# Optimization experiments

Hardware: AMD Instinct MI355X
Metric: run time of the kernel (lower is better)

Reference implementation:

```python
import jax, jax.numpy as jnp
import numpy as np

N = 2048
H_DIM = 64
N_HEADS = 4
N_HIDDEN = H_DIM // N_HEADS  # is_concat=True
L = 16  # max_labels_dim
SLOPE = 0.2


def leaky(x, slope=SLOPE):
    return jnp.where(x >= 0, x, slope * x)


def setup_inputs() -> dict:
    key = jax.random.key(0)
    k1, k2, k3, k4 = jax.random.split(key, 4)
    x = jax.random.normal(k1, (N, H_DIM), dtype=jnp.float32)
    # labels in [0, L]; value == L means unlabeled -> all-zero one-hot row
    lab = jax.random.randint(k2, (N,), 0, L + 1)
    ohm_labels = jnp.where((lab < L)[:, None],
                           jax.nn.one_hot(jnp.minimum(lab, L - 1), L, dtype=jnp.float32),
                           0.0)
    in_features = H_DIM + L
    W_l = jax.random.normal(k3, (H_DIM, in_features), dtype=jnp.float32) / np.sqrt(in_features)
    W_attn = jax.random.normal(k4, (N_HIDDEN,), dtype=jnp.float32) / np.sqrt(N_HIDDEN)
    return {"x": x, "ohm_labels": ohm_labels, "W_l": W_l, "W_attn": W_attn, "sparsity": 0}


def reference(x, ohm_labels, W_l, W_attn, sparsity):
    n_nodes = x.shape[0]
    # fill unlabeled rows with uniform 1/L
    unlabeled = ohm_labels.sum(axis=1) == 0  # (N,)
    ohm = jnp.where(unlabeled[:, None], 1.0 / L, ohm_labels)
    pin = jnp.concatenate([x, ohm], axis=1)  # (N, h_dim + L)

    # shared-weight projection: g_l == g_r == g
    g = (pin @ W_l.T).reshape(n_nodes, N_HEADS, N_HIDDEN)  # (N, H, F)
    # g_sum[i, j] = g_l[j] + g_r[i]  (repeat / repeat_interleave semantics)
    g_sum = g[None, :, :, :] + g[:, None, :, :]            # (N, N, H, F)
    e = jnp.einsum('ijhf,f->ijh', leaky(g_sum), W_attn)    # (N, N, H)
    a = jax.nn.softmax(e, axis=1)                          # softmax over j
    # dropout in eval mode: identity
    attn_res = jnp.einsum('ijh,jhf->ihf', a, g)            # (N, H, F)
    out = attn_res.reshape(n_nodes, N_HEADS * N_HIDDEN)    # is_concat
    h = leaky(out)                                         # processor activation

    # centroids per label from ohm (post-fill) as in get_centroids
    cluster_agg = ohm.T @ h                                # (L, D)
    cnt = ohm.sum(axis=0)                                  # (L,)
    missing = cnt == 0
    centroids = jnp.where(missing[:, None], 0.0,
                          cluster_agg / jnp.where(missing, 1.0, cnt)[:, None])
    # cdist p=2
    diff = h[:, None, :] - centroids[None, :, :]           # (N, L, D)
    scores = -jnp.sqrt(jnp.sum(diff * diff, axis=-1))      # (N, L)
    return scores, h, missing
```

## Files before the change

### kernel.cpp

```cpp
#include <hip/hip_runtime.h>
#include <hip/hip_bf16.h>
#include <math.h>

#define C1F  0.577078016f
#define C2F  0.865617024f

#define WS_CNT 0
#define WS_AGG 128
#define WS_G   8320
#define WS_DCL (8320 + 524288)

typedef float __attribute__((ext_vector_type(4))) f32x4;

__device__ __forceinline__ float rfl(float x) {
    return __uint_as_float(__builtin_amdgcn_readfirstlane(__float_as_uint(x)));
}

__device__ __forceinline__ float dpp_sum(float x) {
    float y;
    y = __int_as_float(__builtin_amdgcn_update_dpp(0, __float_as_int(x), 0x111, 0xf, 0xf, true)); x += y;
    y = __int_as_float(__builtin_amdgcn_update_dpp(0, __float_as_int(x), 0x112, 0xf, 0xf, true)); x += y;
    y = __int_as_float(__builtin_amdgcn_update_dpp(0, __float_as_int(x), 0x114, 0xf, 0xf, true)); x += y;
    y = __int_as_float(__builtin_amdgcn_update_dpp(0, __float_as_int(x), 0x118, 0xf, 0xf, true)); x += y;
    y = __int_as_float(__builtin_amdgcn_update_dpp(0, __float_as_int(x), 0x142, 0xa, 0xf, true)); x += y;
    y = __int_as_float(__builtin_amdgcn_update_dpp(0, __float_as_int(x), 0x143, 0xc, 0xf, true)); x += y;
    return x;
}

__global__ __launch_bounds__(256) void k_proj(
    const float* __restrict__ x, const float* __restrict__ ohm,
    const float* __restrict__ Wl, const float* __restrict__ Wattn,
    unsigned char* __restrict__ ws)
{
    float* g    = (float*)(ws + WS_G);
    float* dclT = (float*)(ws + WS_DCL);
    unsigned long long* cnt = (unsigned long long*)(ws + WS_CNT);

    int t = threadIdx.x;
    int r = blockIdx.x * 4 + (t >> 6);
    int o = t & 63;

    f32x4 oh[4]; float rs = 0.f;
    const f32x4* ohp = (const f32x4*)&ohm[r*16];
    #pragma unroll
    for (int q = 0; q < 4; ++q) { oh[q] = ohp[q]; rs += oh[q][0]+oh[q][1]+oh[q][2]+oh[q][3]; }
    if (rs == 0.f) {
        f32x4 c = {0.0625f, 0.0625f, 0.0625f, 0.0625f};
        #pragma unroll
        for (int q = 0; q < 4; ++q) oh[q] = c;
    }

    float acc = 0.f;
    const f32x4* xp = (const f32x4*)&x[r*64];
    const f32x4* wp = (const f32x4*)&Wl[o*80];
    #pragma unroll
    for (int q = 0; q < 16; ++q) {
        f32x4 a = xp[q], b = wp[q];
        acc = fmaf(a[0],b[0],acc); acc = fmaf(a[1],b[1],acc);
        acc = fmaf(a[2],b[2],acc); acc = fmaf(a[3],b[3],acc);
    }
    #pragma unroll
    for (int q = 0; q < 4; ++q) {
        f32x4 b = wp[16+q];
        acc = fmaf(oh[q][0],b[0],acc); acc = fmaf(oh[q][1],b[1],acc);
        acc = fmaf(oh[q][2],b[2],acc); acc = fmaf(oh[q][3],b[3],acc);
    }
    g[r*64 + o] = acc;

    float dot = Wattn[o & 15] * acc;
    #pragma unroll
    for (int m2 = 1; m2 < 16; m2 <<= 1) dot += __shfl_xor(dot, m2);
    if ((o & 15) == 0) dclT[(o >> 4)*2048 + r] = C2F * dot;

    if (t < 16) {
        float c = 0.f;
        for (int rr = 0; rr < 4; ++rr) {
            int r2 = blockIdx.x*4 + rr; float s = 0.f;
            #pragma unroll
            for (int k = 0; k < 16; ++k) s += ohm[r2*16+k];
            c += (s == 0.f) ? 0.0625f : ohm[r2*16+t];
        }
        atomicAdd(&cnt[t], (unsigned long long)__float2ll_rn(c * 1048576.0f));
    }
}

__global__ __launch_bounds__(512, 3) void k_attn(
    const float* __restrict__ ohm, const float* __restrict__ Wattn,
    unsigned char* __restrict__ ws, float* __restrict__ hout)
{
    float* g    = (float*)(ws + WS_G);
    float* dclT = (float*)(ws + WS_DCL);
    unsigned long long* agg = (unsigned long long*)(ws + WS_AGG);

    __shared__ float gl[128*68];
    __shared__ float shh[256];
    __shared__ float ohmf[64];

    int t = threadIdx.x, bid = blockIdx.x;
    int wid = t >> 6, l = t & 63;
    int rp = wid >> 2, h = wid & 3;
    int i0 = bid*4 + rp*2, i1 = i0 + 1;

    const f32x4* gv4 = (const f32x4*)g;
    float* wbase = &gl[(t >> 4)*68 + (t & 15)*4];

    float wv[16], gA0[16], gA1[16];
    #pragma unroll
    for (int f = 0; f < 16; ++f) wv[f] = rfl(Wattn[f]);
    #pragma unroll
    for (int f = 0; f < 16; ++f) {
        gA0[f] = rfl(g[i0*64 + h*16 + f]);
        gA1[f] = rfl(g[i1*64 + h*16 + f]);
    }

    float acc0[16], acc1[16];
    float l0 = 0.f, l1 = 0.f;
    #pragma unroll
    for (int f = 0; f < 16; ++f) { acc0[f] = 0.f; acc1[f] = 0.f; }

    const float* dpt = dclT + h*2048 + l;

    f32x4 st[4];
    #pragma unroll
    for (int q = 0; q < 4; ++q) st[q] = gv4[t + q*512];
    float djc0 = dpt[0], djc1 = dpt[64];
    float djn0 = 0.f, djn1 = 0.f;

    for (int tile = 0; tile < 16; ++tile) {
        if (tile) __syncthreads();
        #pragma unroll
        for (int q = 0; q < 4; ++q) *(f32x4*)(wbase + q*2176) = st[q];
        __syncthreads();
        if (tile < 15) {
            #pragma unroll
            for (int q = 0; q < 4; ++q) st[q] = gv4[(tile+1)*2048 + t + q*512];
            djn0 = dpt[(tile+1)*128];
            djn1 = dpt[(tile+1)*128 + 64];
        }

        #pragma unroll
        for (int k = 0; k < 2; ++k) {
            const float* gj = &gl[(k*64 + l)*68 + h*16];
            f32x4 q0 = *(const f32x4*)(gj);
            f32x4 q1 = *(const f32x4*)(gj+4);
            f32x4 q2 = *(const f32x4*)(gj+8);
            f32x4 q3 = *(const f32x4*)(gj+12);
            float gvv[16] = { q0[0],q0[1],q0[2],q0[3], q1[0],q1[1],q1[2],q1[3],
                              q2[0],q2[1],q2[2],q2[3], q3[0],q3[1],q3[2],q3[3] };
            float sa0 = 0.f, sb0 = 0.f, sa1 = 0.f, sb1 = 0.f;
            #pragma unroll
            for (int f = 0; f < 16; f += 2) {
                float u0 = gA0[f]   + gvv[f];
                float u1 = gA0[f+1] + gvv[f+1];
                float v0 = gA1[f]   + gvv[f];
                float v1 = gA1[f+1] + gvv[f+1];
                sa0 = fmaf(wv[f],   fabsf(u0), sa0);
                sb0 = fmaf(wv[f+1], fabsf(u1), sb0);
                sa1 = fmaf(wv[f],   fabsf(v0), sa1);
                sb1 = fmaf(wv[f+1], fabsf(v1), sb1);
            }
            float djk = k ? djc1 : djc0;
            float p0 = __builtin_amdgcn_exp2f(fmaf(C1F, sa0 + sb0, djk));
            float p1 = __builtin_amdgcn_exp2f(fmaf(C1F, sa1 + sb1, djk));
            l0 += p0; l1 += p1;
            #pragma unroll
            for (int f = 0; f < 16; ++f) {
                acc0[f] = fmaf(p0, gvv[f], acc0[f]);
                acc1[f] = fmaf(p1, gvv[f], acc1[f]);
            }
        }
        djc0 = djn0; djc1 = djn1;
    }

    float ls0 = dpp_sum(l0), ls1 = dpp_sum(l1);
    float h0[16], h1[16];
    #pragma unroll
    for (int f = 0; f < 16; ++f) { h0[f] = dpp_sum(acc0[f]); h1[f] = dpp_sum(acc1[f]); }

    if (l == 63) {
        float r0 = 1.0f / ls0, r1 = 1.0f / ls1;
        #pragma unroll
        for (int f = 0; f < 16; ++f) {
            float a = h0[f]*r0; a = fmaxf(a, 0.2f*a);
            float b = h1[f]*r1; b = fmaxf(b, 0.2f*b);
            hout[i0*64 + h*16 + f] = a;
            hout[i1*64 + h*16 + f] = b;
            shh[(rp*2    )*64 + h*16 + f] = a;
            shh[(rp*2 + 1)*64 + h*16 + f] = b;
        }
    }
    if (t < 64) {
        int rr = t >> 4, ll = t & 15;
        float v = ohm[(bid*4 + rr)*16 + ll];
        float s = v;
        #pragma unroll
        for (int m2 = 1; m2 < 16; m2 <<= 1) s += __shfl_xor(s, m2);
        ohmf[rr*16 + ll] = (s == 0.f) ? 0.0625f : v;
    }
    __syncthreads();

    for (int v = t; v < 1024; v += 512) {
        int ll = v >> 6, d = v & 63;
        float s = 0.f;
        #pragma unroll
        for (int rr = 0; rr < 4; ++rr) s = fmaf(ohmf[rr*16 + ll], shh[rr*64 + d], s);
        atomicAdd(&agg[v], (unsigned long long)__float2ll_rn(s * 67108864.0f));
    }
}

__global__ __launch_bounds__(256) void k_scores(
    unsigned char* __restrict__ ws, const float* __restrict__ hout,
    float* __restrict__ scores, float* __restrict__ missing)
{
    __shared__ float cl[16*68];
    unsigned long long* cnt = (unsigned long long*)(ws + WS_CNT);
    unsigned long long* agg = (unsigned long long*)(ws + WS_AGG);
    int t = threadIdx.x;

    for (int v = t; v < 1024; v += 256) {
        int ll = v >> 6, d = v & 63;
        long long a = (long long)agg[v];
        long long c = (long long)cnt[ll];
        cl[ll*68 + d] = (c == 0) ? 0.f : ((float)a / (float)c) * 0.015625f;
    }
    if (blockIdx.x == 0 && t < 16) missing[t] = (cnt[t] == 0) ? 1.0f : 0.0f;
    __syncthreads();

    int i = blockIdx.x*16 + (t >> 4), ll = t & 15;
    float s = 0.f;
    #pragma unroll 16
    for (int d = 0; d < 64; ++d) {
        float diff = hout[i*64 + d] - cl[ll*68 + d];
        s = fmaf(diff, diff, s);
    }
    scores[i*16 + ll] = -sqrtf(s);
}

extern "C" void kernel_launch(void* const* d_in, const int* in_sizes, int n_in,
                              void* d_out, int out_size, void* d_ws, size_t ws_size,
                              hipStream_t stream)
{
    const float* x     = (const float*)d_in[0];
    const float* ohm   = (const float*)d_in[1];
    const float* Wl    = (const float*)d_in[2];
    const float* Wattn = (const float*)d_in[3];
    unsigned char* ws  = (unsigned char*)d_ws;

    float* out     = (float*)d_out;
    float* scores  = out;
    float* hout    = out + 2048*16;
    float* missing = out + 2048*16 + 2048*64;

    hipMemsetAsync(d_ws, 0, 8320, stream);
    k_proj  <<<512, 256, 0, stream>>>(x, ohm, Wl, Wattn, ws);
    k_attn  <<<512, 512, 0, stream>>>(ohm, Wattn, ws, hout);
    k_scores<<<128, 256, 0, stream>>>(ws, hout, scores, missing);
}
```

Measured before the change: 63.03 us.

## Transpose g to head-feature-major layout and read it directly from global, dropping LDS tiling

The projection kernel now writes g transposed as [head][feature][node], so each attention thread loads four consecutive j values per feature with vectorized global loads. This removes the shared-memory tile staging and its barriers. Each block now handles two rows with 256 threads across 1024 blocks, and every lane processes four j per pass. This cuts sync and LDS traffic but relies on L2/cache bandwidth for the repeated g reads, and the larger unrolled register set may raise register pressure.

```diff
diff --git a/kernel.cpp b/kernel.cpp
--- a/kernel.cpp
+++ b/kernel.cpp
@@ -32,7 +32,7 @@
     const float* __restrict__ Wl, const float* __restrict__ Wattn,
     unsigned char* __restrict__ ws)
 {
-    float* g    = (float*)(ws + WS_G);
+    float* g2   = (float*)(ws + WS_G);
     float* dclT = (float*)(ws + WS_DCL);
     unsigned long long* cnt = (unsigned long long*)(ws + WS_CNT);
 
@@ -65,7 +65,7 @@
         acc = fmaf(oh[q][0],b[0],acc); acc = fmaf(oh[q][1],b[1],acc);
         acc = fmaf(oh[q][2],b[2],acc); acc = fmaf(oh[q][3],b[3],acc);
     }
-    g[r*64 + o] = acc;
+    g2[(o >> 4)*32768 + (o & 15)*2048 + r] = acc;
 
     float dot = Wattn[o & 15] * acc;
     #pragma unroll
@@ -84,33 +84,30 @@
     }
 }
 
-__global__ __launch_bounds__(512, 3) void k_attn(
+__global__ __launch_bounds__(256, 4) void k_attn(
     const float* __restrict__ ohm, const float* __restrict__ Wattn,
     unsigned char* __restrict__ ws, float* __restrict__ hout)
 {
-    float* g    = (float*)(ws + WS_G);
+    float* g2   = (float*)(ws + WS_G);
     float* dclT = (float*)(ws + WS_DCL);
     unsigned long long* agg = (unsigned long long*)(ws + WS_AGG);
 
-    __shared__ float gl[128*68];
-    __shared__ float shh[256];
-    __shared__ float ohmf[64];
+    __shared__ float shh[128];
+    __shared__ float ohmf[32];
 
     int t = threadIdx.x, bid = blockIdx.x;
-    int wid = t >> 6, l = t & 63;
-    int rp = wid >> 2, h = wid & 3;
-    int i0 = bid*4 + rp*2, i1 = i0 + 1;
-
-    const f32x4* gv4 = (const f32x4*)g;
-    float* wbase = &gl[(t >> 4)*68 + (t & 15)*4];
+    int h = t >> 6, l = t & 63;
+    int i0 = bid*2, i1 = i0 + 1;
+
+    const float* g2h = g2 + h*32768;
+    const float* dpt = dclT + h*2048;
 
     float wv[16], gA0[16], gA1[16];
     #pragma unroll
-    for (int f = 0; f < 16; ++f) wv[f] = rfl(Wattn[f]);
-    #pragma unroll
     for (int f = 0; f < 16; ++f) {
-        gA0[f] = rfl(g[i0*64 + h*16 + f]);
-        gA1[f] = rfl(g[i1*64 + h*16 + f]);
+        wv[f]  = rfl(Wattn[f]);
+        gA0[f] = rfl(g2h[f*2048 + i0]);
+        gA1[f] = rfl(g2h[f*2048 + i1]);
     }
 
     float acc0[16], acc1[16];
@@ -118,58 +115,46 @@
     #pragma unroll
     for (int f = 0; f < 16; ++f) { acc0[f] = 0.f; acc1[f] = 0.f; }
 
-    const float* dpt = dclT + h*2048 + l;
-
-    f32x4 st[4];
-    #pragma unroll
-    for (int q = 0; q < 4; ++q) st[q] = gv4[t + q*512];
-    float djc0 = dpt[0], djc1 = dpt[64];
-    float djn0 = 0.f, djn1 = 0.f;
-
-    for (int tile = 0; tile < 16; ++tile) {
-        if (tile) __syncthreads();
-        #pragma unroll
-        for (int q = 0; q < 4; ++q) *(f32x4*)(wbase + q*2176) = st[q];
-        __syncthreads();
-        if (tile < 15) {
-            #pragma unroll
-            for (int q = 0; q < 4; ++q) st[q] = gv4[(tile+1)*2048 + t + q*512];
-            djn0 = dpt[(tile+1)*128];
-            djn1 = dpt[(tile+1)*128 + 64];
-        }
-
-        #pragma unroll
-        for (int k = 0; k < 2; ++k) {
-            const float* gj = &gl[(k*64 + l)*68 + h*16];
-            f32x4 q0 = *(const f32x4*)(gj);
-            f32x4 q1 = *(const f32x4*)(gj+4);
-            f32x4 q2 = *(const f32x4*)(gj+8);
-            f32x4 q3 = *(const f32x4*)(gj+12);
-            float gvv[16] = { q0[0],q0[1],q0[2],q0[3], q1[0],q1[1],q1[2],q1[3],
-                              q2[0],q2[1],q2[2],q2[3], q3[0],q3[1],q3[2],q3[3] };
-            float sa0 = 0.f, sb0 = 0.f, sa1 = 0.f, sb1 = 0.f;
-            #pragma unroll
-            for (int f = 0; f < 16; f += 2) {
-                float u0 = gA0[f]   + gvv[f];
-                float u1 = gA0[f+1] + gvv[f+1];
-                float v0 = gA1[f]   + gvv[f];
-                float v1 = gA1[f+1] + gvv[f+1];
-                sa0 = fmaf(wv[f],   fabsf(u0), sa0);
-                sb0 = fmaf(wv[f+1], fabsf(u1), sb0);
-                sa1 = fmaf(wv[f],   fabsf(v0), sa1);
-                sb1 = fmaf(wv[f+1], fabsf(v1), sb1);
-            }
-            float djk = k ? djc1 : djc0;
-            float p0 = __builtin_amdgcn_exp2f(fmaf(C1F, sa0 + sb0, djk));
-            float p1 = __builtin_amdgcn_exp2f(fmaf(C1F, sa1 + sb1, djk));
-            l0 += p0; l1 += p1;
-            #pragma unroll
-            for (int f = 0; f < 16; ++f) {
-                acc0[f] = fmaf(p0, gvv[f], acc0[f]);
-                acc1[f] = fmaf(p1, gvv[f], acc1[f]);
-            }
-        }
-        djc0 = djn0; djc1 = djn1;
+    for (int pass = 0; pass < 8; ++pass) {
+        int jb = pass*256 + 4*l;
+        f32x4 G[16];
+        #pragma unroll
+        for (int f = 0; f < 16; ++f) G[f] = *(const f32x4*)&g2h[f*2048 + jb];
+        f32x4 dj = *(const f32x4*)&dpt[jb];
+
+        float e00=0.f,e01=0.f,e02=0.f,e03=0.f;
+        float e10=0.f,e11=0.f,e12=0.f,e13=0.f;
+        #pragma unroll
+        for (int f = 0; f < 16; ++f) {
+            float a0 = gA0[f], a1 = gA1[f];
+            f32x4 gf = G[f];
+            e00 = fmaf(wv[f], fabsf(a0 + gf[0]), e00);
+            e01 = fmaf(wv[f], fabsf(a0 + gf[1]), e01);
+            e02 = fmaf(wv[f], fabsf(a0 + gf[2]), e02);
+            e03 = fmaf(wv[f], fabsf(a0 + gf[3]), e03);
+            e10 = fmaf(wv[f], fabsf(a1 + gf[0]), e10);
+            e11 = fmaf(wv[f], fabsf(a1 + gf[1]), e11);
+            e12 = fmaf(wv[f], fabsf(a1 + gf[2]), e12);
+            e13 = fmaf(wv[f], fabsf(a1 + gf[3]), e13);
+        }
+        float p00 = __builtin_amdgcn_exp2f(fmaf(C1F, e00, dj[0]));
+        float p01 = __builtin_amdgcn_exp2f(fmaf(C1F, e01, dj[1]));
+        float p02 = __builtin_amdgcn_exp2f(fmaf(C1F, e02, dj[2]));
+        float p03 = __builtin_amdgcn_exp2f(fmaf(C1F, e03, dj[3]));
+        float p10 = __builtin_amdgcn_exp2f(fmaf(C1F, e10, dj[0]));
+        float p11 = __builtin_amdgcn_exp2f(fmaf(C1F, e11, dj[1]));
+        float p12 = __builtin_amdgcn_exp2f(fmaf(C1F, e12, dj[2]));
+        float p13 = __builtin_amdgcn_exp2f(fmaf(C1F, e13, dj[3]));
+        l0 += (p00 + p01) + (p02 + p03);
+        l1 += (p10 + p11) + (p12 + p13);
+        #pragma unroll
+        for (int f = 0; f < 16; ++f) {
+            f32x4 gf = G[f];
+            acc0[f] = fmaf(p00, gf[0], fmaf(p01, gf[1],
+                      fmaf(p02, gf[2], fmaf(p03, gf[3], acc0[f]))));
+            acc1[f] = fmaf(p10, gf[0], fmaf(p11, gf[1],
+                      fmaf(p12, gf[2], fmaf(p13, gf[3], acc1[f]))));
+        }
     }
 
     float ls0 = dpp_sum(l0), ls1 = dpp_sum(l1);
@@ -185,13 +170,13 @@
             float b = h1[f]*r1; b = fmaxf(b, 0.2f*b);
             hout[i0*64 + h*16 + f] = a;
             hout[i1*64 + h*16 + f] = b;
-            shh[(rp*2    )*64 + h*16 + f] = a;
-            shh[(rp*2 + 1)*64 + h*16 + f] = b;
-        }
-    }
-    if (t < 64) {
+            shh[       h*16 + f] = a;
+            shh[64 +   h*16 + f] = b;
+        }
+    }
+    if (t < 32) {
         int rr = t >> 4, ll = t & 15;
-        float v = ohm[(bid*4 + rr)*16 + ll];
+        float v = ohm[(bid*2 + rr)*16 + ll];
         float s = v;
         #pragma unroll
         for (int m2 = 1; m2 < 16; m2 <<= 1) s += __shfl_xor(s, m2);
@@ -199,11 +184,9 @@
     }
     __syncthreads();
 
-    for (int v = t; v < 1024; v += 512) {
+    for (int v = t; v < 1024; v += 256) {
         int ll = v >> 6, d = v & 63;
-        float s = 0.f;
-        #pragma unroll
-        for (int rr = 0; rr < 4; ++rr) s = fmaf(ohmf[rr*16 + ll], shh[rr*64 + d], s);
+        float s = fmaf(ohmf[ll], shh[d], ohmf[16 + ll] * shh[64 + d]);
         atomicAdd(&agg[v], (unsigned long long)__float2ll_rn(s * 67108864.0f));
     }
 }
@@ -252,7 +235,7 @@
     float* missing = out + 2048*16 + 2048*64;
 
     hipMemsetAsync(d_ws, 0, 8320, stream);
-    k_proj  <<<512, 256, 0, stream>>>(x, ohm, Wl, Wattn, ws);
-    k_attn  <<<512, 512, 0, stream>>>(ohm, Wattn, ws, hout);
-    k_scores<<<128, 256, 0, stream>>>(ws, hout, scores, missing);
-}
+    k_proj  <<<512,  256, 0, stream>>>(x, ohm, Wl, Wattn, ws);
+    k_attn  <<<1024, 256, 0, stream>>>(ohm, Wattn, ws, hout);
+    k_scores<<<128,  256, 0, stream>>>(ws, hout, scores, missing);
+}
```

Result: slower. 64.68 us (+2.6%).
